# Kernel tuning notes

Measured on AMD Instinct MI355X. Metric: run time of the kernel, lower is better.

Reference implementation:

```python
import jax, jax.numpy as jnp
import numpy as np
import math

B, S, D, H = 2, 2048, 1024, 16
DQ = D // H  # d_qkv = 64


def setup_inputs() -> dict:
    key = jax.random.key(0)
    k1, k2, k3, k4 = jax.random.split(key, 4)
    return {
        "Q": jax.random.normal(k1, (B, S, D), dtype=jnp.float32),
        "K": jax.random.normal(k2, (B, S, D), dtype=jnp.float32),
        "V": jax.random.normal(k3, (B, S, D), dtype=jnp.float32),
        "Wo_w": jax.random.normal(k4, (D, D), dtype=jnp.float32) * 0.02,
        "Wo_b": jnp.zeros((D,), dtype=jnp.float32),
        "mask": 1,
    }


def reference(Q, K, V, Wo_w, Wo_b, mask):
    # Note: original module defines Wq/Wk/Wv but never applies them in forward.
    q = Q.reshape(B, S, H, DQ)
    k = K.reshape(B, S, H, DQ)
    v = V.reshape(B, S, H, DQ)
    # raw QK^T scores: [B, H, S, S]
    scores = jnp.einsum("bqhd,bkhd->bhqk", q, k)
    if mask:
        # torch.triu_indices(S, S) default offset=0 -> mask where key >= query
        # (diagonal included). Fill applied BEFORE the sqrt(d) scaling, as in source.
        tri = jnp.arange(S)[:, None] <= jnp.arange(S)[None, :]  # [S, S]
        scores = jnp.where(tri, jnp.float32(-1e9), scores)
    scale = scores / math.sqrt(DQ)
    attn = jax.nn.softmax(scale, axis=-1)
    ctx = jnp.einsum("bhqk,bkhd->bqhd", attn, v).reshape(B, S, D)
    return ctx @ Wo_w.T + Wo_b
```

## Files before the change

### kernel.cpp

```cpp
#include <hip/hip_runtime.h>
#include <hip/hip_bf16.h>
#include <stdint.h>

#define B_  2
#define S_  2048
#define D_  1024
#define H_  16
#define DQ_ 64
#define QT_ (S_/64)
#define FMAX_ 16.0f

typedef float f32x4 __attribute__((ext_vector_type(4)));
typedef short bf16x8 __attribute__((ext_vector_type(8)));

__device__ __forceinline__ unsigned short f2bf(float f) {
    uint32_t u = __float_as_uint(f);
    u += 0x7fffu + ((u >> 16) & 1u);
    return (unsigned short)(u >> 16);
}
__device__ __forceinline__ float bf2f(unsigned short u) {
    return __uint_as_float(((uint32_t)u) << 16);
}
__device__ __forceinline__ bf16x8 packbf8(float4 a, float4 b) {
    bf16x8 r;
    r[0]=(short)f2bf(a.x); r[1]=(short)f2bf(a.y);
    r[2]=(short)f2bf(a.z); r[3]=(short)f2bf(a.w);
    r[4]=(short)f2bf(b.x); r[5]=(short)f2bf(b.y);
    r[6]=(short)f2bf(b.z); r[7]=(short)f2bf(b.w);
    return r;
}

__global__ __launch_bounds__(256) void prep_kernel(
    const float* __restrict__ K, const float* __restrict__ V,
    const float* __restrict__ W,
    unsigned short* __restrict__ Kb, unsigned short* __restrict__ Vt,
    unsigned short* __restrict__ Wb, float* __restrict__ Pv)
{
    __shared__ unsigned short Ls[64][72];
    const int blk = blockIdx.x, tid = threadIdx.x;

    if (blk < 1024) {
        const int st = blk & 31, h = (blk >> 5) & 15, b = blk >> 9;
        {
            int row = tid >> 2, col0 = (tid & 3) * 16;
            const float* src = V + (((size_t)b*S_ + (size_t)st*64 + row)*D_ + h*64 + col0);
            float4 f0 = ((const float4*)src)[0];
            float4 f1 = ((const float4*)src)[1];
            float4 f2 = ((const float4*)src)[2];
            float4 f3 = ((const float4*)src)[3];
            unsigned short* d = &Ls[row][col0];
            d[0]=f2bf(f0.x); d[1]=f2bf(f0.y); d[2]=f2bf(f0.z); d[3]=f2bf(f0.w);
            d[4]=f2bf(f1.x); d[5]=f2bf(f1.y); d[6]=f2bf(f1.z); d[7]=f2bf(f1.w);
            d[8]=f2bf(f2.x); d[9]=f2bf(f2.y); d[10]=f2bf(f2.z); d[11]=f2bf(f2.w);
            d[12]=f2bf(f3.x); d[13]=f2bf(f3.y); d[14]=f2bf(f3.z); d[15]=f2bf(f3.w);
        }
        __syncthreads();
        {
            int d = tid >> 2, scol = (tid & 3) * 16;
            unsigned short tmp[16];
            float psum = 0.f;
            #pragma unroll
            for (int i = 0; i < 16; ++i) {
                unsigned short u = Ls[scol + i][d];
                tmp[i] = u;
                psum += bf2f(u);
            }
            unsigned short* dst = Vt + ((size_t)((b*H_ + h)*64 + d)*S_ + st*64 + scol);
            ((uint4*)dst)[0] = *((uint4*)tmp);
            ((uint4*)dst)[1] = *((uint4*)(tmp + 8));
            psum += __shfl_xor(psum, 1);
            psum += __shfl_xor(psum, 2);
            if ((tid & 3) == 0)
                Pv[((size_t)(b*H_ + h)*64 + d)*32 + st] = psum;
        }
    } else if (blk < 5120) {
        int i = (blk - 1024)*256 + tid;
        float4 f = ((const float4*)K)[i];
        ushort4 o;
        o.x = f2bf(f.x); o.y = f2bf(f.y); o.z = f2bf(f.z); o.w = f2bf(f.w);
        ((ushort4*)Kb)[i] = o;
    } else {
        int i = (blk - 5120)*256 + tid;
        float4 f = ((const float4*)W)[i];
        ushort4 o;
        o.x = f2bf(f.x); o.y = f2bf(f.y); o.z = f2bf(f.z); o.w = f2bf(f.w);
        ((ushort4*)Wb)[i] = o;
    }
}

__global__ __launch_bounds__(256, 2) void attn_kernel(
    const float* __restrict__ Q,
    const unsigned short* __restrict__ Kb,
    const unsigned short* __restrict__ Vtb,
    const float* __restrict__ Pv,
    unsigned short* __restrict__ ctx,
    const int* __restrict__ maskp)
{
    __shared__ unsigned short Ks [2][64][72];
    __shared__ unsigned short Vts[2][64][72];
    __shared__ unsigned short Ps [4][16][72];

    const int bid = blockIdx.x;
    const int g = bid & 31, pa = bid >> 5;
    const int h = g & 15, b = g >> 4;
    const int tid  = threadIdx.x;
    const int wave = tid >> 6, lane = tid & 63;
    const int quad = lane >> 4, ln = lane & 15;
    const int maskv = maskp[0];

    if (maskv && pa == 0 && tid < 64) {
        const float* p = Pv + ((size_t)(b*H_ + h)*64 + tid)*32;
        float s = 0.f;
        #pragma unroll
        for (int i = 0; i < 32; ++i) s += p[i];
        ctx[(size_t)b*S_*D_ + h*64 + tid] = f2bf(s * (1.0f/S_));
    }

    const int srow = tid >> 2, scol = (tid & 3)*16;
    const unsigned short* kbase =
        Kb + (((size_t)b*S_ + srow)*D_ + h*64 + scol);
    const unsigned short* vbase =
        Vtb + ((size_t)((b*H_ + h)*64 + srow)*S_ + scol);

    for (int t = 0; t < 2; ++t) {
        const int qt = t ? (QT_-1 - pa) : pa;
        const int niter = maskv ? (qt + 1) : QT_;

        const float* qrow =
            Q + (((size_t)b*S_ + (size_t)qt*64 + wave*16 + ln)*D_ + h*64);
        float4 q0 = ((const float4*)(qrow + quad*8))[0];
        float4 q1 = ((const float4*)(qrow + quad*8))[1];
        float4 q2 = ((const float4*)(qrow + 32 + quad*8))[0];
        float4 q3 = ((const float4*)(qrow + 32 + quad*8))[1];
        bf16x8 aq0 = packbf8(q0, q1);
        bf16x8 aq1 = packbf8(q2, q3);

        uint4 k0 = *((const uint4*)(kbase));
        uint4 k1 = *((const uint4*)(kbase + 8));
        uint4 v0 = *((const uint4*)(vbase));
        uint4 v1 = *((const uint4*)(vbase + 8));

        f32x4 o[4] = {};
        float l4[4] = {0.f, 0.f, 0.f, 0.f};
        const int qg = qt*64 + wave*16 + quad*4;

        if (t) __syncthreads();

        for (int j = 0; j < niter; ++j) {
            const int cur = j & 1;
            *((uint4*)&Ks [cur][srow][scol])   = k0;
            *((uint4*)&Ks [cur][srow][scol+8]) = k1;
            *((uint4*)&Vts[cur][srow][scol])   = v0;
            *((uint4*)&Vts[cur][srow][scol+8]) = v1;
            uint4 nk0, nk1, nv0, nv1;
            if (j + 1 < niter) {
                const unsigned short* kp = kbase + (size_t)(j+1)*64*D_;
                const unsigned short* vp = vbase + (j+1)*64;
                nk0 = *((const uint4*)(kp));
                nk1 = *((const uint4*)(kp + 8));
                nv0 = *((const uint4*)(vp));
                nv1 = *((const uint4*)(vp + 8));
            }
            __syncthreads();

            f32x4 s[4] = {};
            #pragma unroll
            for (int nt = 0; nt < 4; ++nt) {
                bf16x8 b0 = *(const bf16x8*)&Ks[cur][nt*16 + ln][quad*8];
                bf16x8 b1 = *(const bf16x8*)&Ks[cur][nt*16 + ln][32 + quad*8];
                s[nt] = __builtin_amdgcn_mfma_f32_16x16x32_bf16(aq0, b0, s[nt], 0,0,0);
                s[nt] = __builtin_amdgcn_mfma_f32_16x16x32_bf16(aq1, b1, s[nt], 0,0,0);
            }

            if (maskv && j == qt) {
                const int kg = j*64 + ln;
                #pragma unroll
                for (int nt = 0; nt < 4; ++nt)
                    #pragma unroll
                    for (int r = 0; r < 4; ++r) {
                        float e = ((kg + nt*16) >= (qg + r)) ? 0.0f
                                   : __expf(s[nt][r]*0.125f - FMAX_);
                        l4[r] += e;
                        Ps[wave][quad*4 + r][nt*16 + ln] = f2bf(e);
                    }
            } else {
                #pragma unroll
                for (int nt = 0; nt < 4; ++nt)
                    #pragma unroll
                    for (int r = 0; r < 4; ++r) {
                        float e = __expf(s[nt][r]*0.125f - FMAX_);
                        l4[r] += e;
                        Ps[wave][quad*4 + r][nt*16 + ln] = f2bf(e);
                    }
            }

            {
                bf16x8 a0 = *(const bf16x8*)&Ps[wave][ln][quad*8];
                bf16x8 a1 = *(const bf16x8*)&Ps[wave][ln][32 + quad*8];
                #pragma unroll
                for (int nt = 0; nt < 4; ++nt) {
                    bf16x8 b0 = *(const bf16x8*)&Vts[cur][nt*16 + ln][quad*8];
                    bf16x8 b1 = *(const bf16x8*)&Vts[cur][nt*16 + ln][32 + quad*8];
                    o[nt] = __builtin_amdgcn_mfma_f32_16x16x32_bf16(a0, b0, o[nt], 0,0,0);
                    o[nt] = __builtin_amdgcn_mfma_f32_16x16x32_bf16(a1, b1, o[nt], 0,0,0);
                }
            }
            k0 = nk0; k1 = nk1; v0 = nv0; v1 = nv1;
        }

        float inv[4];
        #pragma unroll
        for (int r = 0; r < 4; ++r) {
            float lr = l4[r];
            lr += __shfl_xor(lr, 1);
            lr += __shfl_xor(lr, 2);
            lr += __shfl_xor(lr, 4);
            lr += __shfl_xor(lr, 8);
            inv[r] = 1.0f / lr;
        }
        #pragma unroll
        for (int nt = 0; nt < 4; ++nt)
            #pragma unroll
            for (int r = 0; r < 4; ++r) {
                int q = qg + r;
                if (maskv && q == 0) continue;
                int c = h*64 + nt*16 + ln;
                ctx[((size_t)b*S_ + q)*D_ + c] = f2bf(o[nt][r]*inv[r]);
            }
        __syncthreads();
    }
}

__global__ __launch_bounds__(256, 2) void proj_kernel(
    const unsigned short* __restrict__ A,
    const unsigned short* __restrict__ Bw,
    const float* __restrict__ bias,
    float* __restrict__ out)
{
    __shared__ unsigned short As[2][64][72];
    __shared__ unsigned short Bs[2][128][72];
    const int nt0 = blockIdx.x;
    const int mt0 = blockIdx.y;
    const int tid  = threadIdx.x;
    const int wave = tid >> 6, lane = tid & 63;
    const int quad = lane >> 4, ln = lane & 15;

    const int arow = tid >> 2, acol = (tid & 3)*16;
    const int brow = tid >> 1, bcol = (tid & 1)*32;
    const unsigned short* aptr = A  + ((size_t)(mt0*64  + arow)*1024 + acol);
    const unsigned short* bptr = Bw + ((size_t)(nt0*128 + brow)*1024 + bcol);

    uint4 a0 = ((const uint4*)aptr)[0], a1 = ((const uint4*)aptr)[1];
    uint4 b0 = ((const uint4*)bptr)[0], b1 = ((const uint4*)bptr)[1],
          b2 = ((const uint4*)bptr)[2], b3 = ((const uint4*)bptr)[3];

    f32x4 acc[4][2] = {};

    for (int kt = 0; kt < 16; ++kt) {
        const int cur = kt & 1;
        *((uint4*)&As[cur][arow][acol])    = a0;
        *((uint4*)&As[cur][arow][acol+8])  = a1;
        *((uint4*)&Bs[cur][brow][bcol])    = b0;
        *((uint4*)&Bs[cur][brow][bcol+8])  = b1;
        *((uint4*)&Bs[cur][brow][bcol+16]) = b2;
        *((uint4*)&Bs[cur][brow][bcol+24]) = b3;
        uint4 na0, na1, nb0, nb1, nb2, nb3;
        if (kt < 15) {
            const unsigned short* ap = aptr + (kt+1)*64;
            const unsigned short* bp = bptr + (kt+1)*64;
            na0 = ((const uint4*)ap)[0]; na1 = ((const uint4*)ap)[1];
            nb0 = ((const uint4*)bp)[0]; nb1 = ((const uint4*)bp)[1];
            nb2 = ((const uint4*)bp)[2]; nb3 = ((const uint4*)bp)[3];
        }
        __syncthreads();
        #pragma unroll
        for (int ks = 0; ks < 2; ++ks) {
            bf16x8 am[4], bn[2];
            #pragma unroll
            for (int i = 0; i < 4; ++i)
                am[i] = *(const bf16x8*)&As[cur][i*16 + ln][ks*32 + quad*8];
            #pragma unroll
            for (int i = 0; i < 2; ++i)
                bn[i] = *(const bf16x8*)&Bs[cur][wave*32 + i*16 + ln][ks*32 + quad*8];
            #pragma unroll
            for (int mi = 0; mi < 4; ++mi)
                #pragma unroll
                for (int ni = 0; ni < 2; ++ni)
                    acc[mi][ni] = __builtin_amdgcn_mfma_f32_16x16x32_bf16(
                        am[mi], bn[ni], acc[mi][ni], 0,0,0);
        }
        a0 = na0; a1 = na1;
        b0 = nb0; b1 = nb1; b2 = nb2; b3 = nb3;
    }

    #pragma unroll
    for (int mi = 0; mi < 4; ++mi)
        #pragma unroll
        for (int ni = 0; ni < 2; ++ni) {
            int row = mt0*64 + mi*16 + quad*4;
            int col = nt0*128 + wave*32 + ni*16 + ln;
            float bv = bias[col];
            #pragma unroll
            for (int r = 0; r < 4; ++r)
                out[(size_t)(row + r)*1024 + col] = acc[mi][ni][r] + bv;
        }
}

extern "C" void kernel_launch(void* const* d_in, const int* in_sizes, int n_in,
                              void* d_out, int out_size, void* d_ws, size_t ws_size,
                              hipStream_t stream)
{
    const float* Q   = (const float*)d_in[0];
    const float* K   = (const float*)d_in[1];
    const float* V   = (const float*)d_in[2];
    const float* Wo  = (const float*)d_in[3];
    const float* Wb  = (const float*)d_in[4];
    const int* maskp = (const int*)d_in[5];
    float* out = (float*)d_out;

    unsigned short* Kb   = (unsigned short*)d_ws;
    unsigned short* Vtb  = Kb  + (size_t)B_*S_*D_;
    unsigned short* Wob  = Vtb + (size_t)B_*S_*D_;
    unsigned short* ctxb = Wob + (size_t)D_*D_;
    float* Pv = (float*)(ctxb + (size_t)B_*S_*D_);

    prep_kernel<<<6144, 256, 0, stream>>>(K, V, Wo, Kb, Vtb, Wob, Pv);
    attn_kernel<<<512, 256, 0, stream>>>(Q, Kb, Vtb, Pv, ctxb, maskp);
    proj_kernel<<<dim3(8, 64), 256, 0, stream>>>(ctxb, Wob, Wb, out);
}
```

Measured before the change: 156.8 us.

## Load V fragments directly from global, transpose S tile, use exp2 and packed bf16

```diff
diff --git a/kernel.cpp b/kernel.cpp
--- a/kernel.cpp
+++ b/kernel.cpp
@@ -10,6 +10,9 @@
 #define QT_ (S_/64)
 #define FMAX_ 16.0f
 
+#define C1_ 0.18033688011112042f
+#define C0_ (-23.083120654223414f)
+
 typedef float f32x4 __attribute__((ext_vector_type(4)));
 typedef short bf16x8 __attribute__((ext_vector_type(8)));
 
@@ -27,6 +30,18 @@
     r[2]=(short)f2bf(a.z); r[3]=(short)f2bf(a.w);
     r[4]=(short)f2bf(b.x); r[5]=(short)f2bf(b.y);
     r[6]=(short)f2bf(b.z); r[7]=(short)f2bf(b.w);
+    return r;
+}
+__device__ __forceinline__ float fast_exp2(float x) {
+#if __has_builtin(__builtin_amdgcn_exp2f)
+    return __builtin_amdgcn_exp2f(x);
+#else
+    float r; asm("v_exp_f32 %0, %1" : "=v"(r) : "v"(x)); return r;
+#endif
+}
+__device__ __forceinline__ uint32_t cvt_pk_bf16(float lo, float hi) {
+    uint32_t r;
+    asm("v_cvt_pk_bf16_f32 %0, %1, %2" : "=v"(r) : "v"(lo), "v"(hi));
     return r;
 }
 
@@ -97,7 +112,6 @@
     const int* __restrict__ maskp)
 {
     __shared__ unsigned short Ks [2][64][72];
-    __shared__ unsigned short Vts[2][64][72];
     __shared__ unsigned short Ps [4][16][72];
 
     const int bid = blockIdx.x;
@@ -119,8 +133,10 @@
     const int srow = tid >> 2, scol = (tid & 3)*16;
     const unsigned short* kbase =
         Kb + (((size_t)b*S_ + srow)*D_ + h*64 + scol);
-    const unsigned short* vbase =
-        Vtb + ((size_t)((b*H_ + h)*64 + srow)*S_ + scol);
+    const unsigned short* vfb =
+        Vtb + ((size_t)((b*H_ + h)*64 + ln))*S_ + quad*8;
+
+    const int ql = wave*16 + ln;
 
     for (int t = 0; t < 2; ++t) {
         const int qt = t ? (QT_-1 - pa) : pa;
@@ -137,29 +153,31 @@
 
         uint4 k0 = *((const uint4*)(kbase));
         uint4 k1 = *((const uint4*)(kbase + 8));
-        uint4 v0 = *((const uint4*)(vbase));
-        uint4 v1 = *((const uint4*)(vbase + 8));
 
         f32x4 o[4] = {};
-        float l4[4] = {0.f, 0.f, 0.f, 0.f};
+        float lsum = 0.f;
         const int qg = qt*64 + wave*16 + quad*4;
 
         if (t) __syncthreads();
 
         for (int j = 0; j < niter; ++j) {
             const int cur = j & 1;
-            *((uint4*)&Ks [cur][srow][scol])   = k0;
-            *((uint4*)&Ks [cur][srow][scol+8]) = k1;
-            *((uint4*)&Vts[cur][srow][scol])   = v0;
-            *((uint4*)&Vts[cur][srow][scol+8]) = v1;
-            uint4 nk0, nk1, nv0, nv1;
+            *((uint4*)&Ks[cur][srow][scol])   = k0;
+            *((uint4*)&Ks[cur][srow][scol+8]) = k1;
+            uint4 nk0, nk1;
             if (j + 1 < niter) {
                 const unsigned short* kp = kbase + (size_t)(j+1)*64*D_;
-                const unsigned short* vp = vbase + (j+1)*64;
                 nk0 = *((const uint4*)(kp));
                 nk1 = *((const uint4*)(kp + 8));
-                nv0 = *((const uint4*)(vp));
-                nv1 = *((const uint4*)(vp + 8));
+            }
+            bf16x8 vf[4][2];
+            {
+                const unsigned short* vjb = vfb + j*64;
+                #pragma unroll
+                for (int nt = 0; nt < 4; ++nt) {
+                    vf[nt][0] = *(const bf16x8*)(vjb + nt*16*S_);
+                    vf[nt][1] = *(const bf16x8*)(vjb + nt*16*S_ + 32);
+                }
             }
             __syncthreads();
 
@@ -168,30 +186,37 @@
             for (int nt = 0; nt < 4; ++nt) {
                 bf16x8 b0 = *(const bf16x8*)&Ks[cur][nt*16 + ln][quad*8];
                 bf16x8 b1 = *(const bf16x8*)&Ks[cur][nt*16 + ln][32 + quad*8];
-                s[nt] = __builtin_amdgcn_mfma_f32_16x16x32_bf16(aq0, b0, s[nt], 0,0,0);
-                s[nt] = __builtin_amdgcn_mfma_f32_16x16x32_bf16(aq1, b1, s[nt], 0,0,0);
+                s[nt] = __builtin_amdgcn_mfma_f32_16x16x32_bf16(b0, aq0, s[nt], 0,0,0);
+                s[nt] = __builtin_amdgcn_mfma_f32_16x16x32_bf16(b1, aq1, s[nt], 0,0,0);
             }
 
             if (maskv && j == qt) {
-                const int kg = j*64 + ln;
-                #pragma unroll
-                for (int nt = 0; nt < 4; ++nt)
-                    #pragma unroll
-                    for (int r = 0; r < 4; ++r) {
-                        float e = ((kg + nt*16) >= (qg + r)) ? 0.0f
-                                   : __expf(s[nt][r]*0.125f - FMAX_);
-                        l4[r] += e;
-                        Ps[wave][quad*4 + r][nt*16 + ln] = f2bf(e);
-                    }
+                #pragma unroll
+                for (int nt = 0; nt < 4; ++nt) {
+                    const int kl = nt*16 + quad*4;
+                    float e0 = (kl+0 >= ql) ? 0.f : fast_exp2(fmaf(s[nt][0], C1_, C0_));
+                    float e1 = (kl+1 >= ql) ? 0.f : fast_exp2(fmaf(s[nt][1], C1_, C0_));
+                    float e2 = (kl+2 >= ql) ? 0.f : fast_exp2(fmaf(s[nt][2], C1_, C0_));
+                    float e3 = (kl+3 >= ql) ? 0.f : fast_exp2(fmaf(s[nt][3], C1_, C0_));
+                    lsum += (e0+e1)+(e2+e3);
+                    uint2 pk;
+                    pk.x = cvt_pk_bf16(e0, e1);
+                    pk.y = cvt_pk_bf16(e2, e3);
+                    *((uint2*)&Ps[wave][ln][nt*16 + quad*4]) = pk;
+                }
             } else {
                 #pragma unroll
-                for (int nt = 0; nt < 4; ++nt)
-                    #pragma unroll
-                    for (int r = 0; r < 4; ++r) {
-                        float e = __expf(s[nt][r]*0.125f - FMAX_);
-                        l4[r] += e;
-                        Ps[wave][quad*4 + r][nt*16 + ln] = f2bf(e);
-                    }
+                for (int nt = 0; nt < 4; ++nt) {
+                    float e0 = fast_exp2(fmaf(s[nt][0], C1_, C0_));
+                    float e1 = fast_exp2(fmaf(s[nt][1], C1_, C0_));
+                    float e2 = fast_exp2(fmaf(s[nt][2], C1_, C0_));
+                    float e3 = fast_exp2(fmaf(s[nt][3], C1_, C0_));
+                    lsum += (e0+e1)+(e2+e3);
+                    uint2 pk;
+                    pk.x = cvt_pk_bf16(e0, e1);
+                    pk.y = cvt_pk_bf16(e2, e3);
+                    *((uint2*)&Ps[wave][ln][nt*16 + quad*4]) = pk;
+                }
             }
 
             {
@@ -199,25 +224,20 @@
                 bf16x8 a1 = *(const bf16x8*)&Ps[wave][ln][32 + quad*8];
                 #pragma unroll
                 for (int nt = 0; nt < 4; ++nt) {
-                    bf16x8 b0 = *(const bf16x8*)&Vts[cur][nt*16 + ln][quad*8];
-                    bf16x8 b1 = *(const bf16x8*)&Vts[cur][nt*16 + ln][32 + quad*8];
-                    o[nt] = __builtin_amdgcn_mfma_f32_16x16x32_bf16(a0, b0, o[nt], 0,0,0);
-                    o[nt] = __builtin_amdgcn_mfma_f32_16x16x32_bf16(a1, b1, o[nt], 0,0,0);
+                    o[nt] = __builtin_amdgcn_mfma_f32_16x16x32_bf16(a0, vf[nt][0], o[nt], 0,0,0);
+                    o[nt] = __builtin_amdgcn_mfma_f32_16x16x32_bf16(a1, vf[nt][1], o[nt], 0,0,0);
                 }
             }
-            k0 = nk0; k1 = nk1; v0 = nv0; v1 = nv1;
-        }
-
+            k0 = nk0; k1 = nk1;
+        }
+
+        lsum += __shfl_xor(lsum, 16);
+        lsum += __shfl_xor(lsum, 32);
+        float invl = 1.0f / lsum;
         float inv[4];
         #pragma unroll
-        for (int r = 0; r < 4; ++r) {
-            float lr = l4[r];
-            lr += __shfl_xor(lr, 1);
-            lr += __shfl_xor(lr, 2);
-            lr += __shfl_xor(lr, 4);
-            lr += __shfl_xor(lr, 8);
-            inv[r] = 1.0f / lr;
-        }
+        for (int r = 0; r < 4; ++r)
+            inv[r] = __shfl(invl, quad*4 + r);
         #pragma unroll
         for (int nt = 0; nt < 4; ++nt)
             #pragma unroll
```

After: 179.5 us. 14.5% more time.
